# Kernel tuning notes

Measured on AMD Instinct MI355X. Metric: run time of the kernel, lower is better.

## Reference

```python
import jax, jax.numpy as jnp
import numpy as np
from jax import lax

H, W = 512, 1024
C = 34          # Cityscapes label ids; thing classes are 24..33 per Threshold(23.99,50) + <=33
K = 200         # top_k centers kept by NMS
KS = 7          # NMS max-pool kernel
THRESH = 0.1    # NMS score threshold


def setup_inputs() -> dict:
    key = jax.random.key(0)
    k1, k2, k3 = jax.random.split(key, 3)
    return {
        "segmentation_probs": jax.random.normal(k1, (2, C, H, W), jnp.float32),
        "center_maps": jax.random.uniform(k2, (2, 1, H, W), jnp.float32),
        "regression_maps": jax.random.normal(k3, (2, 2, H, W), jnp.float32) * 8.0,
    }


def _nms(center_maps):
    # MaxPool2d(KS, stride=1, pad=KS//2) -> Threshold(0.1, 0) -> keep only local maxima
    pad = KS // 2
    pooled = lax.reduce_window(center_maps, -jnp.inf, lax.max,
                               (1, 1, KS, KS), (1, 1, 1, 1),
                               [(0, 0), (0, 0), (pad, pad), (pad, pad)])
    thresholded = jnp.where(pooled > THRESH, pooled, 0.0)
    # torch: center_map[thresholded != center_map] = 0
    nms_map = jnp.where(thresholded == center_maps, center_maps, 0.0)[:, 0]  # (B,H,W)
    # padded equivalent of nonzero + argsort(desc) + [:top_k]
    probs, idx = lax.top_k(nms_map.reshape(nms_map.shape[0], -1), K)          # (B,K)
    ys, xs = idx // W, idx % W
    return ys, xs, probs, probs > 0.0


def _per_sample(args):
    seg, seg_probs, reg, ys, xs, probs, valid = args
    # --- CreateInstMap: brute-force center-distance argmin ---
    px = (jnp.arange(W, dtype=jnp.float32) + 1.0)[None, :] - reg[0]   # (H,W) pred center x
    py = (jnp.arange(H, dtype=jnp.float32) + 1.0)[:, None] - reg[1]   # (H,W) pred center y
    dx = px[:, :, None] - xs.astype(jnp.float32)[None, None, :]       # (H,W,K)
    dy = py[:, :, None] - ys.astype(jnp.float32)[None, None, :]
    dist2 = dx * dx + dy * dy            # argmin(sqrt(d2)) == argmin(d2); sqrt omitted safely
    dist2 = jnp.where(valid[None, None, :], dist2, jnp.inf)           # ignore padded centers
    closest = jnp.argmin(dist2, -1).astype(jnp.int32) + 1             # (H,W), ids in 1..K
    # --- SeperateInstMap: thing mask, per-instance majority class / mean prob ---
    things = (seg >= 24) & (seg <= 33)   # Threshold(23.99,50) then <= 33
    inst_ids = jnp.where(things, closest, 0)                          # 0 = background/stuff
    flat_ids = inst_ids.reshape(-1)
    comb = flat_ids * C + seg.reshape(-1)                             # joint (inst, class) id
    counts = jax.ops.segment_sum(jnp.ones(H * W, jnp.float32), comb,
                                 num_segments=(K + 1) * C).reshape(K + 1, C)[1:]   # (K,C)
    sums = jax.ops.segment_sum(seg_probs.reshape(C, -1).T, flat_ids,
                               num_segments=K + 1)[1:]                # (K,C) prob sums per inst
    n = counts.sum(-1)                                                # (K,) pixels per instance
    inst_class = jnp.argmax(counts, -1).astype(jnp.int32)             # majority seg class
    s = jnp.take_along_axis(sums, inst_class[:, None], axis=1)[:, 0]
    seg_prob = jnp.where(n > 0, s / jnp.maximum(n, 1.0), 0.0)         # mean seg prob over mask
    return inst_class, probs, seg_prob, n.astype(jnp.int32), (n > 0) & valid, closest


def reference(segmentation_probs, center_maps, regression_maps):
    seg_probs = jax.nn.softmax(segmentation_probs, axis=1)
    segs = jnp.argmax(segmentation_probs, axis=1).astype(jnp.int32)   # (B,H,W)
    ys, xs, probs, valid = _nms(center_maps)
    # sequential over batch (mirrors python loop, bounds peak memory of (H,W,K) field)
    inst_class, inst_prob, seg_prob, n_pix, valid_inst, closest = lax.map(
        _per_sample, (segs, seg_probs, regression_maps, ys, xs, probs, valid))
    return inst_class, inst_prob, seg_prob, n_pix, valid_inst, segs, closest
```

## Files before the change

kernel.cpp:

```cpp
#include <hip/hip_runtime.h>
#include <stdint.h>

#define NB 2
#define NC 34
#define HH 512
#define WW 1024
#define HWW (HH*WW)
#define KK 200
#define MCAP 4096
#define VBIN 4096
#define SLOTS 256
#define NTILE 256
#define SEGB (NB*HWW/1024)
#define NMSB (NB*NTILE)
#define STRIP 4096
#define SUMB (NB*HWW/STRIP)

#define TW 128
#define TH 16
#define HALO 3

__global__ void __launch_bounds__(256)
k_seg_nms(const float* __restrict__ logits, const float* __restrict__ cmap,
          float* __restrict__ segs_out, float* __restrict__ scomb,
          unsigned char* __restrict__ seg8,
          uint64_t* __restrict__ cand, uint32_t* __restrict__ tcnt,
          int use_stats) {
    int bid = blockIdx.x;
    int tid = threadIdx.x;

    if (bid < SEGB) {
        int t = bid * 256 + tid;
        int p = t * 4;
        int b = p / HWW, r = p - b * HWW;
        const float* base = logits + (size_t)b * NC * HWW + r;
        float4 m = make_float4(-3e38f, -3e38f, -3e38f, -3e38f);
        float4 s = make_float4(0.f, 0.f, 0.f, 0.f);
        int ax = 0, ay = 0, az = 0, aw = 0;
#pragma unroll
        for (int c = 0; c < NC; ++c) {
            float4 v = *(const float4*)(base + (size_t)c * HWW);
            if (v.x > m.x) { s.x = s.x * __expf(m.x - v.x) + 1.f; m.x = v.x; ax = c; }
            else            s.x += __expf(v.x - m.x);
            if (v.y > m.y) { s.y = s.y * __expf(m.y - v.y) + 1.f; m.y = v.y; ay = c; }
            else            s.y += __expf(v.y - m.y);
            if (v.z > m.z) { s.z = s.z * __expf(m.z - v.z) + 1.f; m.z = v.z; az = c; }
            else            s.z += __expf(v.z - m.z);
            if (v.w > m.w) { s.w = s.w * __expf(m.w - v.w) + 1.f; m.w = v.w; aw = c; }
            else            s.w += __expf(v.w - m.w);
        }
        *(float4*)(segs_out + p) = make_float4((float)ax, (float)ay, (float)az, (float)aw);
        *(uchar4*)(seg8 + p) = make_uchar4((unsigned char)ax, (unsigned char)ay,
                                           (unsigned char)az, (unsigned char)aw);
        if (use_stats) {
            *(float4*)(scomb + p) = make_float4(m.x + __logf(s.x), m.y + __logf(s.y),
                                                m.z + __logf(s.z), m.w + __logf(s.w));
        }
        return;
    }

    __shared__ float sIn[TH + 2 * HALO][TW + 2 * HALO];
    __shared__ float sH[TH + 2 * HALO][TW];
    __shared__ uint64_t lc[SLOTS];
    __shared__ uint32_t lcnt;
    int t2 = bid - SEGB;
    int bx = t2 & (WW / TW - 1);
    int by = (t2 >> 3) & (HH / TH - 1);
    int b = t2 >> 8;
    int tb = t2 & (NTILE - 1);
    const float* bb = cmap + (size_t)b * HWW;
    if (tid == 0) lcnt = 0u;

    const int LW = TW + 2 * HALO;
    const int LH = TH + 2 * HALO;
    for (int idx = tid; idx < LW * LH; idx += 256) {
        int r = idx / LW, c = idx - r * LW;
        int gh = by * TH + r - HALO;
        int gw = bx * TW + c - HALO;
        float v = -3e38f;
        if (gh >= 0 && gh < HH && gw >= 0 && gw < WW) v = bb[gh * WW + gw];
        sIn[r][c] = v;
    }
    __syncthreads();
    for (int idx = tid; idx < LH * TW; idx += 256) {
        int r = idx / TW, c = idx - r * TW;
        float m = fmaxf(fmaxf(fmaxf(sIn[r][c], sIn[r][c + 1]),
                              fmaxf(sIn[r][c + 2], sIn[r][c + 3])),
                        fmaxf(fmaxf(sIn[r][c + 4], sIn[r][c + 5]), sIn[r][c + 6]));
        sH[r][c] = m;
    }
    __syncthreads();
    for (int idx = tid; idx < TH * TW; idx += 256) {
        int r = idx >> 7, c = idx & (TW - 1);
        float cv = sIn[r + HALO][c + HALO];
        float m = fmaxf(fmaxf(fmaxf(sH[r][c], sH[r + 1][c]),
                              fmaxf(sH[r + 2][c], sH[r + 3][c])),
                        fmaxf(fmaxf(sH[r + 4][c], sH[r + 5][c]), sH[r + 6][c]));
        if (m > 0.1f && cv == m) {
            int gh = by * TH + r;
            int gw = bx * TW + c;
            uint32_t rr = (uint32_t)(gh * WW + gw);
            uint32_t pos = atomicAdd(&lcnt, 1u);
            if (pos < SLOTS)
                lc[pos] = ((uint64_t)__float_as_uint(cv) << 32) |
                          (uint64_t)(0xFFFFFFFFu - rr);
        }
    }
    __syncthreads();
    uint32_t n = lcnt;
    if (n > SLOTS) n = SLOTS;
    uint64_t* cslot = cand + ((size_t)(b * NTILE + tb)) * SLOTS;
    for (uint32_t i = tid; i < n; i += 256) cslot[i] = lc[i];
    if (tid == 0) tcnt[b * NTILE + tb] = n;
}

__global__ void __launch_bounds__(1024) k_topk2(const uint64_t* __restrict__ cand,
                                                const uint32_t* __restrict__ tcnt,
                                                float* __restrict__ probs_out,
                                                float* __restrict__ cxy,
                                                uint32_t* __restrict__ counts,
                                                float* __restrict__ sums,
                                                uint32_t* __restrict__ done) {
    int b = blockIdx.x;
    int tid = threadIdx.x;
    int lane = tid & 63, wv = tid >> 6;
    __shared__ uint32_t hist[VBIN];
    __shared__ uint32_t part[1024];
    __shared__ uint32_t wsum[16];
    __shared__ uint32_t ltc[NTILE];
    __shared__ uint64_t lkey[MCAP];
    __shared__ uint32_t lM;
    __shared__ int sBstar;

    {
        uint32_t* zc = counts + (size_t)b * (KK + 1) * NC;
        for (int i = tid; i < (KK + 1) * NC; i += 1024) zc[i] = 0u;
        float* zs = sums + b * (KK + 1);
        for (int i = tid; i < KK + 1; i += 1024) zs[i] = 0.f;
        if (b == 0 && tid == 0) done[0] = 0u;
    }
    if (tid < KK) {
        probs_out[b * KK + tid] = 0.f;
        cxy[(b * KK + tid) * 2]     = 1e19f;
        cxy[(b * KK + tid) * 2 + 1] = 1e19f;
    }
    if (tid == 0) { lM = 0u; sBstar = 0; }
    if (tid < NTILE) ltc[tid] = tcnt[b * NTILE + tid];
    for (int i = tid; i < VBIN; i += 1024) hist[i] = 0u;
    __syncthreads();

    const uint64_t* cb = cand + (size_t)b * NTILE * SLOTS;
    int tile = tid >> 2, l4 = tid & 3;
    uint32_t n_t = ltc[tile];

    for (uint32_t sl = l4; sl < n_t; sl += 4) {
        uint64_t kk = cb[tile * SLOTS + sl];
        float v = __uint_as_float((uint32_t)(kk >> 32));
        int bin = (int)(v * (float)VBIN);
        bin = bin < 0 ? 0 : (bin > VBIN - 1 ? VBIN - 1 : bin);
        atomicAdd(&hist[bin], 1u);
    }
    __syncthreads();

    int base = VBIN - 4 * (tid + 1);
    uint32_t s = hist[base] + hist[base + 1] + hist[base + 2] + hist[base + 3];
    uint32_t sc = s;
#pragma unroll
    for (int off = 1; off < 64; off <<= 1) {
        uint32_t nv = __shfl_up(sc, off, 64);
        if (lane >= off) sc += nv;
    }
    if (lane == 63) wsum[wv] = sc;
    __syncthreads();
    if (wv == 0) {
        uint32_t t0 = (lane < 16) ? wsum[lane] : 0u;
#pragma unroll
        for (int off = 1; off < 16; off <<= 1) {
            uint32_t nv = __shfl_up(t0, off, 64);
            if (lane >= off) t0 += nv;
        }
        if (lane < 16) wsum[lane] = t0;
    }
    __syncthreads();
    uint32_t inc = sc + (wv > 0 ? wsum[wv - 1] : 0u);
    part[tid] = inc;
    __syncthreads();
    {
        uint32_t Pt = part[tid];
        uint32_t Pp = (tid > 0) ? part[tid - 1] : 0u;
        if (Pt >= KK && Pp < KK) {
            uint32_t cum = Pp;
            int bs = base;
            for (int j = base + 3; j >= base; --j) {
                cum += hist[j];
                if (cum >= KK) { bs = j; break; }
            }
            sBstar = bs;
        }
    }
    __syncthreads();
    int bstar = sBstar;

    for (uint32_t sl = l4; sl < n_t; sl += 4) {
        uint64_t kk = cb[tile * SLOTS + sl];
        float v = __uint_as_float((uint32_t)(kk >> 32));
        int bin = (int)(v * (float)VBIN);
        bin = bin < 0 ? 0 : (bin > VBIN - 1 ? VBIN - 1 : bin);
        if (bin >= bstar) {
            uint32_t pos = atomicAdd(&lM, 1u);
            if (pos < MCAP) lkey[pos] = kk;
        }
    }
    __syncthreads();
    uint32_t M = lM;
    if (M > MCAP) M = MCAP;
    for (uint32_t i = tid; i < M; i += 1024) {
        uint64_t kk = lkey[i];
        uint32_t rank = 0;
        for (uint32_t j = 0; j < M; ++j) rank += (lkey[j] > kk) ? 1u : 0u;
        if (rank < KK) {
            uint32_t bits = (uint32_t)(kk >> 32);
            uint32_t idx = 0xFFFFFFFFu - (uint32_t)(kk & 0xFFFFFFFFull);
            probs_out[b * KK + rank] = __uint_as_float(bits);
            cxy[(b * KK + rank) * 2]     = (float)(idx % WW);
            cxy[(b * KK + rank) * 2 + 1] = (float)(idx / WW);
        }
    }
}

__global__ void __launch_bounds__(256) k_assign(const float* __restrict__ reg,
                                                const float* __restrict__ cxy,
                                                const unsigned char* __restrict__ seg8,
                                                float* __restrict__ closest_out,
                                                uint16_t* __restrict__ aux,
                                                uint32_t* __restrict__ counts) {
    __shared__ float2 cc[KK];
    __shared__ float4 ccs[KK];
    __shared__ float sred[4][4];
    __shared__ uint32_t wcnt[4];
    __shared__ float stau2;
    __shared__ uint32_t sS;

    int t = blockIdx.x;
    int tx = t & 63;
    int ty = (t >> 6) & 31;
    int b = t >> 11;
    int tid = threadIdx.x;
    int lane = tid & 63, wv = tid >> 6;
    int w = tx * 16 + (tid & 15);
    int h = ty * 16 + (tid >> 4);
    int r = h * WW + w;
    int p = b * HWW + r;

    if (tid < KK) cc[tid] = ((const float2*)cxy)[b * KK + tid];
    __syncthreads();

    float rx = reg[(size_t)b * 2 * HWW + r];
    float ry = reg[(size_t)b * 2 * HWW + HWW + r];
    float px = (float)(w + 1) - rx;
    float py = (float)(h + 1) - ry;

    float mnx = px, mxx = px, mny = py, mxy = py;
#pragma unroll
    for (int off = 1; off < 64; off <<= 1) {
        mnx = fminf(mnx, __shfl_xor(mnx, off, 64));
        mxx = fmaxf(mxx, __shfl_xor(mxx, off, 64));
        mny = fminf(mny, __shfl_xor(mny, off, 64));
        mxy = fmaxf(mxy, __shfl_xor(mxy, off, 64));
    }
    if (lane == 0) { sred[0][wv] = mnx; sred[1][wv] = mxx; sred[2][wv] = mny; sred[3][wv] = mxy; }
    __syncthreads();
    float xmin = fminf(fminf(sred[0][0], sred[0][1]), fminf(sred[0][2], sred[0][3]));
    float xmax = fmaxf(fmaxf(sred[1][0], sred[1][1]), fmaxf(sred[1][2], sred[1][3]));
    float ymin = fminf(fminf(sred[2][0], sred[2][1]), fminf(sred[2][2], sred[2][3]));
    float ymax = fmaxf(fmaxf(sred[3][0], sred[3][1]), fmaxf(sred[3][2], sred[3][3]));

    float2 c0 = cc[tid < KK ? tid : 0];
    float mdx = fmaxf(fmaxf(xmin - c0.x, c0.x - xmax), 0.f);
    float mdy = fmaxf(fmaxf(ymin - c0.y, c0.y - ymax), 0.f);
    float mind2 = mdx * mdx + mdy * mdy;
    float Mdx = fmaxf(c0.x - xmin, xmax - c0.x);
    float Mdy = fmaxf(c0.y - ymin, ymax - c0.y);
    float maxd2 = Mdx * Mdx + Mdy * Mdy;

    float v = (tid < KK) ? maxd2 : 3.0e38f;
#pragma unroll
    for (int off = 1; off < 64; off <<= 1) v = fminf(v, __shfl_xor(v, off, 64));
    if (lane == 0) sred[0][wv] = v;
    __syncthreads();
    if (tid == 0) {
        float mm = fminf(fminf(sred[0][0], sred[0][1]), fminf(sred[0][2], sred[0][3]));
        float tau = __builtin_sqrtf(mm) + 1.0f;
        stau2 = tau * tau;
    }
    __syncthreads();

    bool flag = (tid < KK) && (mind2 <= stau2);
    uint64_t mask = __ballot(flag);
    uint32_t myoff = (uint32_t)__popcll(mask & ((1ull << lane) - 1ull));
    if (lane == 0) wcnt[wv] = (uint32_t)__popcll(mask);
    __syncthreads();
    uint32_t pre = 0;
    for (int i = 0; i < wv; ++i) pre += wcnt[i];
    if (flag) ccs[pre + myoff] = make_float4(c0.x, c0.y, (float)tid, 0.f);
    if (tid == 0) sS = wcnt[0] + wcnt[1] + wcnt[2] + wcnt[3];
    __syncthreads();
    uint32_t S = sS;

    float best = __builtin_inff();
    float bkf = 0.f;
    for (uint32_t s = 0; s < S; ++s) {
        float4 c = ccs[s];
        float dx = __fsub_rn(px, c.x);
        float dy = __fsub_rn(py, c.y);
        float d2 = __fadd_rn(__fmul_rn(dx, dx), __fmul_rn(dy, dy));
        if (d2 < best) { best = d2; bkf = c.z; }
    }
    int bk = (int)bkf;
    closest_out[p] = bkf + 1.0f;
    int seg = (int)seg8[p];
    aux[p] = (uint16_t)(((bk + 1) << 6) | seg);
    if (seg >= 24 && seg <= 33) {
        atomicAdd(&counts[(b * (KK + 1) + (bk + 1)) * NC + seg], 1u);
    }
}

template <int USE_STATS>
__global__ void __launch_bounds__(256) k_sums(const float* __restrict__ logits,
                                              const uint16_t* __restrict__ aux,
                                              const float* __restrict__ scomb,
                                              const uint32_t* __restrict__ counts,
                                              const float* __restrict__ probs_out,
                                              float* __restrict__ sums,
                                              float* __restrict__ ic_out,
                                              float* __restrict__ np_out,
                                              float* __restrict__ va_out,
                                              float* __restrict__ sp_out,
                                              uint32_t* __restrict__ done) {
    __shared__ int ic_l[KK];
    __shared__ float psum[KK + 1];
    __shared__ uint32_t sticket;
    int tid = threadIdx.x;
    int sblk = blockIdx.x;
    int b = sblk / (HWW / STRIP);
    int p0 = sblk * STRIP;

    if (tid < KK) {
        const uint32_t* row = counts + (size_t)(b * (KK + 1) + (tid + 1)) * NC;
        uint32_t n = 0, mx = 0;
        int am = 0;
#pragma unroll
        for (int c = 0; c < NC; ++c) {
            uint32_t x = row[c];
            n += x;
            if (x > mx) { mx = x; am = c; }
        }
        ic_l[tid] = am;
        if ((sblk % (HWW / STRIP)) == 0) {
            ic_out[b * KK + tid] = (float)am;
            np_out[b * KK + tid] = (float)n;
            va_out[b * KK + tid] =
                (n > 0u && probs_out[b * KK + tid] > 0.f) ? 1.f : 0.f;
        }
    }
    if (tid < KK + 1) psum[tid] = 0.f;
    __syncthreads();

#pragma unroll 1
    for (int ch = 0; ch < STRIP / 512; ++ch) {
        int p = p0 + ch * 512 + tid * 2;
        int r = p - b * HWW;
        uint32_t a2 = *(const uint32_t*)(aux + p);
        int seg0 = (int)(a2 & 63u), seg1 = (int)((a2 >> 16) & 63u);
        bool th0 = (seg0 >= 24) & (seg0 <= 33);
        bool th1 = (seg1 >= 24) & (seg1 <= 33);
        float2 sc = make_float2(0.f, 0.f);
        if (USE_STATS && (th0 || th1)) sc = *(const float2*)(scomb + p);
        const float* base = logits + (size_t)b * NC * HWW + r;
#pragma unroll
        for (int j = 0; j < 2; ++j) {
            bool th = j ? th1 : th0;
            if (th) {
                uint32_t pk = (a2 >> (16 * j)) & 0xFFFFu;
                int cl = (int)(pk >> 6);
                int ic = ic_l[cl - 1];
                float pr;
                if (USE_STATS) {
                    float lv = base[(size_t)ic * HWW + j];
                    pr = __expf(lv - (j ? sc.y : sc.x));
                } else {
                    float vmax = -3e38f, lv = 0.f, s = 0.f;
                    float vv[NC];
#pragma unroll
                    for (int c = 0; c < NC; ++c) {
                        vv[c] = base[(size_t)c * HWW + j];
                        vmax = fmaxf(vmax, vv[c]);
                        if (c == ic) lv = vv[c];
                    }
#pragma unroll
                    for (int c = 0; c < NC; ++c) s += __expf(vv[c] - vmax);
                    pr = __expf(lv - vmax) / s;
                }
                atomicAdd(&psum[cl], pr);
            }
        }
    }
    __syncthreads();
    if (tid < KK + 1) {
        float x = psum[tid];
        if (x != 0.f) atomicAdd(&sums[b * (KK + 1) + tid], x);
    }
    __threadfence();
    __syncthreads();
    if (tid == 0) sticket = atomicAdd(&done[0], 1u);
    __syncthreads();
    if (sticket == (uint32_t)SUMB - 1u) {
        __threadfence();
        for (int t = tid; t < NB * KK; t += 256) {
            int bb = t / KK, k = t - bb * KK;
            const uint32_t* row = counts + (size_t)(bb * (KK + 1) + (k + 1)) * NC;
            uint32_t n = 0;
#pragma unroll
            for (int c = 0; c < NC; ++c) n += row[c];
            float s2 = atomicAdd(&sums[bb * (KK + 1) + k + 1], 0.f);
            sp_out[t] = (n > 0u) ? (s2 / (float)n) : 0.f;
        }
    }
}

extern "C" void kernel_launch(void* const* d_in, const int* in_sizes, int n_in,
                              void* d_out, int out_size, void* d_ws, size_t ws_size,
                              hipStream_t stream) {
    const float* logits = (const float*)d_in[0];
    const float* cmap   = (const float*)d_in[1];
    const float* reg    = (const float*)d_in[2];
    float* out = (float*)d_out;
    float* o_ic   = out;
    float* o_prob = out + NB * KK;
    float* o_sp   = out + 2 * NB * KK;
    float* o_np   = out + 3 * NB * KK;
    float* o_va   = out + 4 * NB * KK;
    float* o_segs = out + 5 * NB * KK;
    float* o_clo  = out + 5 * NB * KK + NB * HWW;

    char* w = (char*)d_ws;
    size_t off = 0;
    auto alloc = [&](size_t bytes) {
        off = (off + 15) & ~((size_t)15);
        void* p = w + off;
        off += bytes;
        return p;
    };
    uint64_t* cand   = (uint64_t*)alloc(sizeof(uint64_t) * NB * NTILE * SLOTS);
    uint32_t* tcnt   = (uint32_t*)alloc(sizeof(uint32_t) * NB * NTILE);
    uint32_t* counts = (uint32_t*)alloc(sizeof(uint32_t) * NB * (KK + 1) * NC);
    float* sums      = (float*)alloc(sizeof(float) * NB * (KK + 1));
    uint32_t* done   = (uint32_t*)alloc(sizeof(uint32_t) * 4);
    float* cxy       = (float*)alloc(sizeof(float) * NB * KK * 2);
    unsigned char* seg8 = (unsigned char*)alloc(sizeof(unsigned char) * NB * HWW);
    uint16_t* aux    = (uint16_t*)alloc(sizeof(uint16_t) * NB * HWW);
    size_t base_need = (off + 15) & ~((size_t)15);
    float* scomb = (float*)(w + base_need);
    int use_stats = (base_need + sizeof(float) * (size_t)NB * HWW) <= ws_size ? 1 : 0;

    k_seg_nms<<<SEGB + NMSB, 256, 0, stream>>>(logits, cmap, o_segs, scomb, seg8,
                                               cand, tcnt, use_stats);
    k_topk2<<<NB, 1024, 0, stream>>>(cand, tcnt, o_prob, cxy, counts, sums, done);
    k_assign<<<NB * 2048, 256, 0, stream>>>(reg, cxy, seg8, o_clo, aux, counts);
    if (use_stats)
        k_sums<1><<<SUMB, 256, 0, stream>>>(logits, aux, scomb, counts, o_prob,
                                            sums, o_ic, o_np, o_va, o_sp, done);
    else
        k_sums<0><<<SUMB, 256, 0, stream>>>(logits, aux, scomb, counts, o_prob,
                                            sums, o_ic, o_np, o_va, o_sp, done);
}
```

Measured before the change: 102.0 us.

## Overlap top-k selection with part of the segmentation pass across kernels

The segmentation argmax/softmax-stat work is split between two kernels. The first kernel runs NMS tiles plus 768 seg chunks. The second runs the 2 top-k blocks alongside the remaining seg chunks, so the small serial top-k kernel no longer occupies the GPU alone. Top-k is reshaped to 256 threads with one tile per thread and 16 histogram bins per thread, and MCAP is halved to shrink shared memory. Zeroing of counts/sums/done moves into the NMS blocks via a contiguous workspace region. The risk is that the two top-k blocks become the tail of the second kernel, and that a smaller MCAP could overflow on heavy ties.

```diff
diff --git a/kernel.cpp b/kernel.cpp
--- a/kernel.cpp
+++ b/kernel.cpp
@@ -7,63 +7,80 @@
 #define WW 1024
 #define HWW (HH*WW)
 #define KK 200
-#define MCAP 4096
+#define MCAP 2048
 #define VBIN 4096
 #define SLOTS 256
 #define NTILE 256
-#define SEGB (NB*HWW/1024)
+#define SEGT (NB*HWW/1024)
+#define SEGA 768
+#define SEGB2 (SEGT - SEGA)
 #define NMSB (NB*NTILE)
 #define STRIP 4096
 #define SUMB (NB*HWW/STRIP)
+#define ZW (NB*(KK+1)*NC + NB*(KK+1) + 4)
 
 #define TW 128
 #define TH 16
 #define HALO 3
 
+__device__ __forceinline__ void seg_body(int chunk, int tid,
+                                         const float* __restrict__ logits,
+                                         float* __restrict__ segs_out,
+                                         float* __restrict__ scomb,
+                                         unsigned char* __restrict__ seg8,
+                                         int use_stats) {
+    int t = chunk * 256 + tid;
+    int p = t * 4;
+    int b = p / HWW, r = p - b * HWW;
+    const float* base = logits + (size_t)b * NC * HWW + r;
+    float4 m = make_float4(-3e38f, -3e38f, -3e38f, -3e38f);
+    float4 s = make_float4(0.f, 0.f, 0.f, 0.f);
+    int ax = 0, ay = 0, az = 0, aw = 0;
+#pragma unroll
+    for (int c = 0; c < NC; ++c) {
+        float4 v = *(const float4*)(base + (size_t)c * HWW);
+        if (v.x > m.x) { s.x = s.x * __expf(m.x - v.x) + 1.f; m.x = v.x; ax = c; }
+        else            s.x += __expf(v.x - m.x);
+        if (v.y > m.y) { s.y = s.y * __expf(m.y - v.y) + 1.f; m.y = v.y; ay = c; }
+        else            s.y += __expf(v.y - m.y);
+        if (v.z > m.z) { s.z = s.z * __expf(m.z - v.z) + 1.f; m.z = v.z; az = c; }
+        else            s.z += __expf(v.z - m.z);
+        if (v.w > m.w) { s.w = s.w * __expf(m.w - v.w) + 1.f; m.w = v.w; aw = c; }
+        else            s.w += __expf(v.w - m.w);
+    }
+    *(float4*)(segs_out + p) = make_float4((float)ax, (float)ay, (float)az, (float)aw);
+    *(uchar4*)(seg8 + p) = make_uchar4((unsigned char)ax, (unsigned char)ay,
+                                       (unsigned char)az, (unsigned char)aw);
+    if (use_stats) {
+        *(float4*)(scomb + p) = make_float4(m.x + __logf(s.x), m.y + __logf(s.y),
+                                            m.z + __logf(s.z), m.w + __logf(s.w));
+    }
+}
+
 __global__ void __launch_bounds__(256)
-k_seg_nms(const float* __restrict__ logits, const float* __restrict__ cmap,
-          float* __restrict__ segs_out, float* __restrict__ scomb,
-          unsigned char* __restrict__ seg8,
-          uint64_t* __restrict__ cand, uint32_t* __restrict__ tcnt,
-          int use_stats) {
+k_a(const float* __restrict__ logits, const float* __restrict__ cmap,
+    float* __restrict__ segs_out, float* __restrict__ scomb,
+    unsigned char* __restrict__ seg8,
+    uint64_t* __restrict__ cand, uint32_t* __restrict__ tcnt,
+    uint32_t* __restrict__ zbase, int use_stats) {
     int bid = blockIdx.x;
     int tid = threadIdx.x;
 
-    if (bid < SEGB) {
-        int t = bid * 256 + tid;
-        int p = t * 4;
-        int b = p / HWW, r = p - b * HWW;
-        const float* base = logits + (size_t)b * NC * HWW + r;
-        float4 m = make_float4(-3e38f, -3e38f, -3e38f, -3e38f);
-        float4 s = make_float4(0.f, 0.f, 0.f, 0.f);
-        int ax = 0, ay = 0, az = 0, aw = 0;
-#pragma unroll
-        for (int c = 0; c < NC; ++c) {
-            float4 v = *(const float4*)(base + (size_t)c * HWW);
-            if (v.x > m.x) { s.x = s.x * __expf(m.x - v.x) + 1.f; m.x = v.x; ax = c; }
-            else            s.x += __expf(v.x - m.x);
-            if (v.y > m.y) { s.y = s.y * __expf(m.y - v.y) + 1.f; m.y = v.y; ay = c; }
-            else            s.y += __expf(v.y - m.y);
-            if (v.z > m.z) { s.z = s.z * __expf(m.z - v.z) + 1.f; m.z = v.z; az = c; }
-            else            s.z += __expf(v.z - m.z);
-            if (v.w > m.w) { s.w = s.w * __expf(m.w - v.w) + 1.f; m.w = v.w; aw = c; }
-            else            s.w += __expf(v.w - m.w);
-        }
-        *(float4*)(segs_out + p) = make_float4((float)ax, (float)ay, (float)az, (float)aw);
-        *(uchar4*)(seg8 + p) = make_uchar4((unsigned char)ax, (unsigned char)ay,
-                                           (unsigned char)az, (unsigned char)aw);
-        if (use_stats) {
-            *(float4*)(scomb + p) = make_float4(m.x + __logf(s.x), m.y + __logf(s.y),
-                                                m.z + __logf(s.z), m.w + __logf(s.w));
-        }
+    if (bid >= NMSB) {
+        seg_body(bid - NMSB, tid, logits, segs_out, scomb, seg8, use_stats);
         return;
+    }
+
+    {
+        int i = bid * 256 + tid;
+        if (i < ZW) zbase[i] = 0u;
     }
 
     __shared__ float sIn[TH + 2 * HALO][TW + 2 * HALO];
     __shared__ float sH[TH + 2 * HALO][TW];
     __shared__ uint64_t lc[SLOTS];
     __shared__ uint32_t lcnt;
-    int t2 = bid - SEGB;
+    int t2 = bid;
     int bx = t2 & (WW / TW - 1);
     int by = (t2 >> 3) & (HH / TH - 1);
     int b = t2 >> 8;
@@ -114,56 +131,70 @@
     if (tid == 0) tcnt[b * NTILE + tb] = n;
 }
 
-__global__ void __launch_bounds__(1024) k_topk2(const uint64_t* __restrict__ cand,
-                                                const uint32_t* __restrict__ tcnt,
-                                                float* __restrict__ probs_out,
-                                                float* __restrict__ cxy,
-                                                uint32_t* __restrict__ counts,
-                                                float* __restrict__ sums,
-                                                uint32_t* __restrict__ done) {
-    int b = blockIdx.x;
+__global__ void __launch_bounds__(256)
+k_b(const float* __restrict__ logits, const uint64_t* __restrict__ cand,
+    const uint32_t* __restrict__ tcnt,
+    float* __restrict__ segs_out, float* __restrict__ scomb,
+    unsigned char* __restrict__ seg8,
+    float* __restrict__ probs_out, float* __restrict__ cxy, int use_stats) {
+    int bid = blockIdx.x;
     int tid = threadIdx.x;
+
+    if (bid >= NB) {
+        seg_body(SEGA + (bid - NB), tid, logits, segs_out, scomb, seg8, use_stats);
+        return;
+    }
+
+    int b = bid;
     int lane = tid & 63, wv = tid >> 6;
     __shared__ uint32_t hist[VBIN];
-    __shared__ uint32_t part[1024];
-    __shared__ uint32_t wsum[16];
+    __shared__ uint32_t part[256];
+    __shared__ uint32_t wsum[4];
     __shared__ uint32_t ltc[NTILE];
     __shared__ uint64_t lkey[MCAP];
     __shared__ uint32_t lM;
     __shared__ int sBstar;
 
-    {
-        uint32_t* zc = counts + (size_t)b * (KK + 1) * NC;
-        for (int i = tid; i < (KK + 1) * NC; i += 1024) zc[i] = 0u;
-        float* zs = sums + b * (KK + 1);
-        for (int i = tid; i < KK + 1; i += 1024) zs[i] = 0.f;
-        if (b == 0 && tid == 0) done[0] = 0u;
-    }
     if (tid < KK) {
         probs_out[b * KK + tid] = 0.f;
         cxy[(b * KK + tid) * 2]     = 1e19f;
         cxy[(b * KK + tid) * 2 + 1] = 1e19f;
     }
     if (tid == 0) { lM = 0u; sBstar = 0; }
-    if (tid < NTILE) ltc[tid] = tcnt[b * NTILE + tid];
-    for (int i = tid; i < VBIN; i += 1024) hist[i] = 0u;
+    ltc[tid] = tcnt[b * NTILE + tid];
+    for (int i = tid; i < VBIN; i += 256) hist[i] = 0u;
     __syncthreads();
 
     const uint64_t* cb = cand + (size_t)b * NTILE * SLOTS;
-    int tile = tid >> 2, l4 = tid & 3;
-    uint32_t n_t = ltc[tile];
-
-    for (uint32_t sl = l4; sl < n_t; sl += 4) {
-        uint64_t kk = cb[tile * SLOTS + sl];
-        float v = __uint_as_float((uint32_t)(kk >> 32));
-        int bin = (int)(v * (float)VBIN);
-        bin = bin < 0 ? 0 : (bin > VBIN - 1 ? VBIN - 1 : bin);
-        atomicAdd(&hist[bin], 1u);
-    }
-    __syncthreads();
-
-    int base = VBIN - 4 * (tid + 1);
-    uint32_t s = hist[base] + hist[base + 1] + hist[base + 2] + hist[base + 3];
+    const uint64_t* tp = cb + (size_t)tid * SLOTS;
+    uint32_t n_t = ltc[tid];
+
+    {
+        uint32_t sl = 0;
+        for (; sl + 4 <= n_t; sl += 4) {
+            uint64_t k0 = tp[sl], k1 = tp[sl + 1], k2 = tp[sl + 2], k3 = tp[sl + 3];
+#pragma unroll
+            for (int j = 0; j < 4; ++j) {
+                uint64_t kk = j == 0 ? k0 : (j == 1 ? k1 : (j == 2 ? k2 : k3));
+                float v = __uint_as_float((uint32_t)(kk >> 32));
+                int bin = (int)(v * (float)VBIN);
+                bin = bin < 0 ? 0 : (bin > VBIN - 1 ? VBIN - 1 : bin);
+                atomicAdd(&hist[bin], 1u);
+            }
+        }
+        for (; sl < n_t; ++sl) {
+            float v = __uint_as_float((uint32_t)(tp[sl] >> 32));
+            int bin = (int)(v * (float)VBIN);
+            bin = bin < 0 ? 0 : (bin > VBIN - 1 ? VBIN - 1 : bin);
+            atomicAdd(&hist[bin], 1u);
+        }
+    }
+    __syncthreads();
+
+    int base = VBIN - 16 * (tid + 1);
+    uint32_t s = 0;
+#pragma unroll
+    for (int j = 0; j < 16; ++j) s += hist[base + j];
     uint32_t sc = s;
 #pragma unroll
     for (int off = 1; off < 64; off <<= 1) {
@@ -172,17 +203,9 @@
     }
     if (lane == 63) wsum[wv] = sc;
     __syncthreads();
-    if (wv == 0) {
-        uint32_t t0 = (lane < 16) ? wsum[lane] : 0u;
-#pragma unroll
-        for (int off = 1; off < 16; off <<= 1) {
-            uint32_t nv = __shfl_up(t0, off, 64);
-            if (lane >= off) t0 += nv;
-        }
-        if (lane < 16) wsum[lane] = t0;
-    }
-    __syncthreads();
-    uint32_t inc = sc + (wv > 0 ? wsum[wv - 1] : 0u);
+    uint32_t pre = 0;
+    for (int i = 0; i < wv; ++i) pre += wsum[i];
+    uint32_t inc = sc + pre;
     part[tid] = inc;
     __syncthreads();
     {
@@ -191,7 +214,7 @@
         if (Pt >= KK && Pp < KK) {
             uint32_t cum = Pp;
             int bs = base;
-            for (int j = base + 3; j >= base; --j) {
+            for (int j = base + 15; j >= base; --j) {
                 cum += hist[j];
                 if (cum >= KK) { bs = j; break; }
             }
@@ -201,8 +224,8 @@
     __syncthreads();
     int bstar = sBstar;
 
-    for (uint32_t sl = l4; sl < n_t; sl += 4) {
-        uint64_t kk = cb[tile * SLOTS + sl];
+    for (uint32_t sl = 0; sl < n_t; ++sl) {
+        uint64_t kk = tp[sl];
         float v = __uint_as_float((uint32_t)(kk >> 32));
         int bin = (int)(v * (float)VBIN);
         bin = bin < 0 ? 0 : (bin > VBIN - 1 ? VBIN - 1 : bin);
@@ -214,7 +237,7 @@
     __syncthreads();
     uint32_t M = lM;
     if (M > MCAP) M = MCAP;
-    for (uint32_t i = tid; i < M; i += 1024) {
+    for (uint32_t i = tid; i < M; i += 256) {
         uint64_t kk = lkey[i];
         uint32_t rank = 0;
         for (uint32_t j = 0; j < M; ++j) rank += (lkey[j] > kk) ? 1u : 0u;
@@ -451,11 +474,13 @@
         off += bytes;
         return p;
     };
+    uint32_t* zbase  = (uint32_t*)alloc(sizeof(uint32_t) * ZW);
+    uint32_t* counts = zbase;
+    float*    sums   = (float*)(counts + NB * (KK + 1) * NC);
+    uint32_t* done   = (uint32_t*)(sums + NB * (KK + 1));
+
     uint64_t* cand   = (uint64_t*)alloc(sizeof(uint64_t) * NB * NTILE * SLOTS);
     uint32_t* tcnt   = (uint32_t*)alloc(sizeof(uint32_t) * NB * NTILE);
-    uint32_t* counts = (uint32_t*)alloc(sizeof(uint32_t) * NB * (KK + 1) * NC);
-    float* sums      = (float*)alloc(sizeof(float) * NB * (KK + 1));
-    uint32_t* done   = (uint32_t*)alloc(sizeof(uint32_t) * 4);
     float* cxy       = (float*)alloc(sizeof(float) * NB * KK * 2);
     unsigned char* seg8 = (unsigned char*)alloc(sizeof(unsigned char) * NB * HWW);
     uint16_t* aux    = (uint16_t*)alloc(sizeof(uint16_t) * NB * HWW);
@@ -463,9 +488,10 @@
     float* scomb = (float*)(w + base_need);
     int use_stats = (base_need + sizeof(float) * (size_t)NB * HWW) <= ws_size ? 1 : 0;
 
-    k_seg_nms<<<SEGB + NMSB, 256, 0, stream>>>(logits, cmap, o_segs, scomb, seg8,
-                                               cand, tcnt, use_stats);
-    k_topk2<<<NB, 1024, 0, stream>>>(cand, tcnt, o_prob, cxy, counts, sums, done);
+    k_a<<<NMSB + SEGA, 256, 0, stream>>>(logits, cmap, o_segs, scomb, seg8,
+                                         cand, tcnt, zbase, use_stats);
+    k_b<<<NB + SEGB2, 256, 0, stream>>>(logits, cand, tcnt, o_segs, scomb, seg8,
+                                        o_prob, cxy, use_stats);
     k_assign<<<NB * 2048, 256, 0, stream>>>(reg, cxy, seg8, o_clo, aux, counts);
     if (use_stats)
         k_sums<1><<<SUMB, 256, 0, stream>>>(logits, aux, scomb, counts, o_prob,
```

After: 112.0 us. +9.8%, slower.
